# Kernel tuning notes

Hardware: AMD Instinct MI355X
Metric: run time of the kernel (lower is better)

Reference implementation:

```python
import jax, jax.numpy as jnp
import numpy as np

PARENTS = (-1, 0, 0, 0, 1, 2, 3, 4, 5, 6, 7, 8, 9, 9, 9, 12, 13, 14, 16, 17, 18, 19, 20, 21)
NUM_JOINTS = 24
ROT_RANGE = 0.2
SCALE_RANGE = 0.1
CAM_JIT = 0.1
IMG_SIZE = 512.0
EPS = 1e-8


def _rodrigues(axis, angle):
    # axis: [B,3] (will be re-normalized as in the torch code), angle: [B]
    axis = axis / (jnp.linalg.norm(axis, axis=1, keepdims=True) + EPS)
    c = jnp.cos(angle)[:, None, None]
    s = jnp.sin(angle)[:, None, None]
    x, y, z = axis[:, 0], axis[:, 1], axis[:, 2]
    zeros = jnp.zeros_like(x)
    K = jnp.stack([
        jnp.stack([zeros, -z, y], axis=1),
        jnp.stack([z, zeros, -x], axis=1),
        jnp.stack([-y, x, zeros], axis=1),
    ], axis=1)  # [B,3,3]
    I = jnp.eye(3, dtype=axis.dtype)[None]
    outer = axis[:, :, None] * axis[:, None, :]
    return I + s * K + (1.0 - c) * (outer - I)


def setup_inputs() -> dict:
    key = jax.random.key(0)
    ks = jax.random.split(key, 12)
    B, J = 131072, NUM_JOINTS
    return {
        'poses_3d': jax.random.normal(ks[0], (B, J, 3), jnp.float32),
        'rot_mats': jax.random.normal(ks[1], (B, J, 3, 3), jnp.float32),
        'axis': jax.random.normal(ks[2], (B, J, 3), jnp.float32),
        'angle_u': jax.random.uniform(ks[3], (B, J), jnp.float32),
        'scale_u': jax.random.uniform(ks[4], (B, J), jnp.float32),
        'K': jax.random.normal(ks[5], (B, 3, 3), jnp.float32),
        'R': jax.random.normal(ks[6], (B, 3, 3), jnp.float32),
        't': jax.random.normal(ks[7], (B, 3), jnp.float32),
        'focal_u': jax.random.uniform(ks[8], (B, 2), jnp.float32),
        'yaw_u': jax.random.uniform(ks[9], (B,), jnp.float32),
        'pitch_u': jax.random.uniform(ks[10], (B,), jnp.float32),
        't_jit': jax.random.normal(ks[11], (B, 3), jnp.float32),
    }


def reference(poses_3d, rot_mats, axis, angle_u, scale_u, K, R, t, focal_u, yaw_u, pitch_u, t_jit):
    poses = poses_3d
    rots = rot_mats
    # sequential kinematic-tree walk (parents[i] < i, so already-updated parents feed children)
    for i in range(1, NUM_JOINTS):
        p = PARENTS[i]
        bone = poses[:, i] - poses[:, p]                                   # [B,3]
        blen = jnp.linalg.norm(bone, axis=1, keepdims=True)
        ax = axis[:, i]
        ax = ax / (jnp.linalg.norm(ax, axis=1, keepdims=True) + EPS)       # first normalization (forward)
        ang = (angle_u[:, i] * 2.0 - 1.0) * ROT_RANGE
        Ra = _rodrigues(ax, ang)                                           # [B,3,3]
        rb = jnp.einsum('bij,bj->bi', Ra, bone)
        scale = 1.0 + (scale_u[:, i:i + 1] * 2.0 - 1.0) * SCALE_RANGE
        nb = rb * scale * blen / (jnp.linalg.norm(rb, axis=1, keepdims=True) + EPS)
        poses = poses.at[:, i].set(poses[:, p] + nb)
        rots = rots.at[:, i].set(jnp.einsum('bij,bjk->bik', rots[:, i], Ra))

    # camera jitter
    fs = 1.0 + (focal_u * 2.0 - 1.0) * CAM_JIT * 0.1                       # [B,2]
    K_aug = K.at[:, 0, 0].set(K[:, 0, 0] * fs[:, 0]).at[:, 1, 1].set(K[:, 1, 1] * fs[:, 1])
    yaw = (yaw_u * 2.0 - 1.0) * CAM_JIT * 0.1
    pitch = (pitch_u * 2.0 - 1.0) * CAM_JIT * 0.05
    cy, sy = jnp.cos(yaw), jnp.sin(yaw)
    cp, sp = jnp.cos(pitch), jnp.sin(pitch)
    z = jnp.zeros_like(cy)
    o = jnp.ones_like(cy)
    R_yaw = jnp.stack([jnp.stack([cy, z, sy], 1), jnp.stack([z, o, z], 1), jnp.stack([-sy, z, cy], 1)], 1)
    R_pitch = jnp.stack([jnp.stack([o, z, z], 1), jnp.stack([z, cp, -sp], 1), jnp.stack([z, sp, cp], 1)], 1)
    R_aug = jnp.einsum('bij,bjk->bik', R, jnp.einsum('bij,bjk->bik', R_yaw, R_pitch))
    t_aug = t + t_jit * CAM_JIT * 0.05

    # project and normalize
    cam = jnp.einsum('bij,bnj->bni', R_aug, poses) + t_aug[:, None, :]     # [B,J,3]
    zc = jnp.maximum(cam[:, :, 2], 1e-5)
    u = K_aug[:, 0, 0][:, None] * (cam[:, :, 0] / zc) + K_aug[:, 0, 2][:, None]
    v = K_aug[:, 1, 1][:, None] * (cam[:, :, 1] / zc) + K_aug[:, 1, 2][:, None]
    poses_2d = jnp.stack([u, v], axis=2) / IMG_SIZE * 2.0 - 1.0

    return poses, poses_2d, rots, K_aug, R_aug, t_aug
```

## Files before the change

### kernel.cpp

```cpp
#include <hip/hip_runtime.h>

#define NJ 24
#define EPSF 1e-8f

static __device__ __forceinline__ int parent_of(int i) {
    constexpr int P[NJ] = {-1, 0, 0, 0, 1, 2, 3, 4, 5, 6, 7, 8, 9, 9, 9, 12, 13, 14, 16, 17, 18, 19, 20, 21};
    return P[i];
}

static __device__ __forceinline__ void make_Ra(float ax, float ay, float az, float au, float R[9]) {
    float n1 = sqrtf(ax*ax + ay*ay + az*az) + EPSF;
    ax /= n1; ay /= n1; az /= n1;
    float n2 = sqrtf(ax*ax + ay*ay + az*az) + EPSF;
    ax /= n2; ay /= n2; az /= n2;
    float ang = (au * 2.0f - 1.0f) * 0.2f;
    float c = cosf(ang), s = sinf(ang), oc = 1.0f - c;
    R[0] = 1.0f + oc*(ax*ax - 1.0f); R[1] = -s*az + oc*ax*ay;        R[2] =  s*ay + oc*ax*az;
    R[3] =  s*az + oc*ax*ay;         R[4] = 1.0f + oc*(ay*ay - 1.0f); R[5] = -s*ax + oc*ay*az;
    R[6] = -s*ay + oc*ax*az;         R[7] =  s*ax + oc*ay*az;         R[8] = 1.0f + oc*(az*az - 1.0f);
}

__global__ __launch_bounds__(64)
void poseaug_fused_kernel(const float* __restrict__ poses_3d,
                          const float* __restrict__ rot_mats,
                          const float* __restrict__ axis,
                          const float* __restrict__ angle_u,
                          const float* __restrict__ scale_u,
                          const float* __restrict__ Kin,
                          const float* __restrict__ Rin,
                          const float* __restrict__ tin,
                          const float* __restrict__ focal_u,
                          const float* __restrict__ yaw_u,
                          const float* __restrict__ pitch_u,
                          const float* __restrict__ t_jit,
                          float* __restrict__ out, int B)
{
    __shared__ __align__(16) float stg[64 * 73];
    __shared__ __align__(16) float rbuf[64 * 73];
    const int l  = threadIdx.x;
    const int e0 = blockIdx.x * 64;
    const int n  = min(64, B - e0);
    const int b  = e0 + l;
    const bool act = (b < B);

    float* out_poses = out;
    float* out_2d    = out + (size_t)B * 72;
    float* out_rots  = out + (size_t)B * 120;
    float* out_K     = out + (size_t)B * 336;
    float* out_R     = out + (size_t)B * 345;
    float* out_t     = out + (size_t)B * 354;

    {
        const float* gp = poses_3d + (size_t)e0 * 72;
        const float* ga = axis     + (size_t)e0 * 72;
        if (n == 64) {
            const float4* gp4 = (const float4*)gp;
            const float4* ga4 = (const float4*)ga;
            #pragma unroll
            for (int it = 0; it < 18; ++it) {
                int i4 = l + it * 64;
                float4 vp = gp4[i4];
                float4 va = ga4[i4];
                int o = i4 * 4;
                int base = (o / 72) * 73 + (o % 72);
                rbuf[base] = vp.x; rbuf[base+1] = vp.y; rbuf[base+2] = vp.z; rbuf[base+3] = vp.w;
                stg[base]  = va.x; stg[base+1]  = va.y; stg[base+2]  = va.z; stg[base+3]  = va.w;
            }
        } else {
            for (int o = l; o < n * 72; o += 64) {
                int base = (o / 72) * 73 + (o % 72);
                rbuf[base] = gp[o];
                stg[base]  = ga[o];
            }
        }
    }
    __syncthreads();
    float pf[72];
    #pragma unroll
    for (int k = 0; k < 72; ++k) pf[k] = rbuf[l * 73 + k];

    float au[24], su[24];
    if (act) {
        const float4* ga = (const float4*)(angle_u + (size_t)b * 24);
        const float4* gs = (const float4*)(scale_u + (size_t)b * 24);
        #pragma unroll
        for (int q = 0; q < 6; ++q) {
            float4 va = ga[q]; au[4*q+0]=va.x; au[4*q+1]=va.y; au[4*q+2]=va.z; au[4*q+3]=va.w;
            float4 vs = gs[q]; su[4*q+0]=vs.x; su[4*q+1]=vs.y; su[4*q+2]=vs.z; su[4*q+3]=vs.w;
        }
    }

    #pragma unroll
    for (int i = 1; i < NJ; ++i) {
        const int par = parent_of(i);
        float bx = pf[3*i+0] - pf[3*par+0];
        float by = pf[3*i+1] - pf[3*par+1];
        float bz = pf[3*i+2] - pf[3*par+2];
        float blen = sqrtf(bx*bx + by*by + bz*bz);

        float Ra[9];
        make_Ra(stg[l*73 + 3*i + 0], stg[l*73 + 3*i + 1], stg[l*73 + 3*i + 2], au[i], Ra);

        float rbx = Ra[0]*bx + Ra[1]*by + Ra[2]*bz;
        float rby = Ra[3]*bx + Ra[4]*by + Ra[5]*bz;
        float rbz = Ra[6]*bx + Ra[7]*by + Ra[8]*bz;

        float scale = 1.0f + (su[i] * 2.0f - 1.0f) * 0.1f;
        float rn = sqrtf(rbx*rbx + rby*rby + rbz*rbz) + EPSF;
        float f = scale * blen / rn;

        pf[3*i+0] = pf[3*par+0] + rbx * f;
        pf[3*i+1] = pf[3*par+1] + rby * f;
        pf[3*i+2] = pf[3*par+2] + rbz * f;
    }

    float K00, K02, K11, K12;
    float A[9], tx = 0.f, ty = 0.f, tz = 0.f;
    if (act) {
        float Kf[9];
        const float* kb = Kin + (size_t)b * 9;
        const float* rb = Rin + (size_t)b * 9;
        #pragma unroll
        for (int k = 0; k < 9; ++k) Kf[k] = kb[k];
        float f0 = focal_u[(size_t)b*2+0], f1 = focal_u[(size_t)b*2+1];
        Kf[0] *= 1.0f + (f0*2.0f - 1.0f) * 0.01f;
        Kf[4] *= 1.0f + (f1*2.0f - 1.0f) * 0.01f;
        K00 = Kf[0]; K02 = Kf[2]; K11 = Kf[4]; K12 = Kf[5];

        float yaw   = (yaw_u[b]   * 2.0f - 1.0f) * 0.01f;
        float pitch = (pitch_u[b] * 2.0f - 1.0f) * 0.005f;
        float cy = cosf(yaw),  sy = sinf(yaw);
        float cp = cosf(pitch), sp = sinf(pitch);
        float M00 = cy,   M01 = sy*sp, M02 = sy*cp;
        float M11 = cp,   M12 = -sp;
        float M20 = -sy,  M21 = cy*sp, M22 = cy*cp;

        float R00=rb[0],R01=rb[1],R02=rb[2],R10=rb[3],R11=rb[4],R12=rb[5],R20=rb[6],R21=rb[7],R22=rb[8];
        A[0] = R00*M00 + R02*M20; A[1] = R00*M01 + R01*M11 + R02*M21; A[2] = R00*M02 + R01*M12 + R02*M22;
        A[3] = R10*M00 + R12*M20; A[4] = R10*M01 + R11*M11 + R12*M21; A[5] = R10*M02 + R11*M12 + R12*M22;
        A[6] = R20*M00 + R22*M20; A[7] = R20*M01 + R21*M11 + R22*M21; A[8] = R20*M02 + R21*M12 + R22*M22;

        tx = tin[(size_t)b*3+0] + t_jit[(size_t)b*3+0] * 0.005f;
        ty = tin[(size_t)b*3+1] + t_jit[(size_t)b*3+1] * 0.005f;
        tz = tin[(size_t)b*3+2] + t_jit[(size_t)b*3+2] * 0.005f;

        float* ok = out_K + (size_t)b * 9;
        #pragma unroll
        for (int k = 0; k < 9; ++k) ok[k] = Kf[k];
        float* orr = out_R + (size_t)b * 9;
        #pragma unroll
        for (int k = 0; k < 9; ++k) orr[k] = A[k];
        float* ot = out_t + (size_t)b * 3;
        ot[0] = tx; ot[1] = ty; ot[2] = tz;
    }

    #pragma unroll
    for (int c = 0; c < 3; ++c) {
        __syncthreads();
        const float* gld = rot_mats + (size_t)e0 * 216 + 72 * c;
        if (n == 64) {
            #pragma unroll
            for (int it = 0; it < 18; ++it) {
                int f = it * 64 + l;
                int r = f / 18;
                int k = (f % 18) * 4;
                const float4 v = *(const float4*)(gld + (size_t)r * 216 + k);
                int base = r * 73 + k;
                rbuf[base] = v.x; rbuf[base+1] = v.y; rbuf[base+2] = v.z; rbuf[base+3] = v.w;
            }
        } else {
            for (int o = l; o < n * 72; o += 64)
                rbuf[(o/72)*73 + (o%72)] = gld[(size_t)(o/72)*216 + (o%72)];
        }
        __syncthreads();
        if (act) {
            #pragma unroll
            for (int jj = 0; jj < 8; ++jj) {
                const int j = c * 8 + jj;
                float m[9];
                #pragma unroll
                for (int q = 0; q < 9; ++q) m[q] = rbuf[l*73 + 9*jj + q];
                float r9[9];
                if (j == 0) {
                    #pragma unroll
                    for (int q = 0; q < 9; ++q) r9[q] = m[q];
                } else {
                    float Ra[9];
                    make_Ra(stg[l*73 + 3*j + 0], stg[l*73 + 3*j + 1], stg[l*73 + 3*j + 2], au[j], Ra);
                    r9[0] = m[0]*Ra[0] + m[1]*Ra[3] + m[2]*Ra[6];
                    r9[1] = m[0]*Ra[1] + m[1]*Ra[4] + m[2]*Ra[7];
                    r9[2] = m[0]*Ra[2] + m[1]*Ra[5] + m[2]*Ra[8];
                    r9[3] = m[3]*Ra[0] + m[4]*Ra[3] + m[5]*Ra[6];
                    r9[4] = m[3]*Ra[1] + m[4]*Ra[4] + m[5]*Ra[7];
                    r9[5] = m[3]*Ra[2] + m[4]*Ra[5] + m[5]*Ra[8];
                    r9[6] = m[6]*Ra[0] + m[7]*Ra[3] + m[8]*Ra[6];
                    r9[7] = m[6]*Ra[1] + m[7]*Ra[4] + m[8]*Ra[7];
                    r9[8] = m[6]*Ra[2] + m[7]*Ra[5] + m[8]*Ra[8];
                }
                #pragma unroll
                for (int q = 0; q < 9; ++q) rbuf[l*73 + 9*jj + q] = r9[q];
            }
        }
        __syncthreads();
        float* gst = out_rots + (size_t)e0 * 216 + 72 * c;
        if (n == 64) {
            #pragma unroll
            for (int it = 0; it < 18; ++it) {
                int f = it * 64 + l;
                int r = f / 18;
                int k = (f % 18) * 4;
                int base = r * 73 + k;
                *(float4*)(gst + (size_t)r * 216 + k) =
                    make_float4(rbuf[base], rbuf[base+1], rbuf[base+2], rbuf[base+3]);
            }
        } else {
            for (int o = l; o < n * 72; o += 64)
                gst[(size_t)(o/72)*216 + (o%72)] = rbuf[(o/72)*73 + (o%72)];
        }
    }

    __syncthreads();
    #pragma unroll
    for (int k = 0; k < 72; ++k) stg[l * 73 + k] = pf[k];
    __syncthreads();
    {
        float* g = out_poses + (size_t)e0 * 72;
        if (n == 64) {
            float4* g4 = (float4*)g;
            #pragma unroll
            for (int it = 0; it < 18; ++it) {
                int i4 = l + it * 64;
                int o = i4 * 4;
                int base = (o / 72) * 73 + (o % 72);
                g4[i4] = make_float4(stg[base], stg[base+1], stg[base+2], stg[base+3]);
            }
        } else {
            for (int o = l; o < n * 72; o += 64) g[o] = stg[(o / 72) * 73 + (o % 72)];
        }
    }

    __syncthreads();
    if (act) {
        #pragma unroll
        for (int j = 0; j < NJ; ++j) {
            float px = pf[3*j+0], py = pf[3*j+1], pz = pf[3*j+2];
            float cx = A[0]*px + A[1]*py + A[2]*pz + tx;
            float cv = A[3]*px + A[4]*py + A[5]*pz + ty;
            float cz = A[6]*px + A[7]*py + A[8]*pz + tz;
            float zc = fmaxf(cz, 1e-5f);
            stg[l*73 + 2*j + 0] = (K00 * (cx / zc) + K02) * (2.0f / 512.0f) - 1.0f;
            stg[l*73 + 2*j + 1] = (K11 * (cv / zc) + K12) * (2.0f / 512.0f) - 1.0f;
        }
    }
    __syncthreads();
    {
        float* g = out_2d + (size_t)e0 * 48;
        if (n == 64) {
            float4* g4 = (float4*)g;
            #pragma unroll
            for (int it = 0; it < 12; ++it) {
                int i4 = l + it * 64;
                int o = i4 * 4;
                int base = (o / 48) * 73 + (o % 48);
                g4[i4] = make_float4(stg[base], stg[base+1], stg[base+2], stg[base+3]);
            }
        } else {
            for (int o = l; o < n * 48; o += 64) g[o] = stg[(o / 48) * 73 + (o % 48)];
        }
    }
}

extern "C" void kernel_launch(void* const* d_in, const int* in_sizes, int n_in,
                              void* d_out, int out_size, void* d_ws, size_t ws_size,
                              hipStream_t stream) {
    const float* poses_3d = (const float*)d_in[0];
    const float* rot_mats = (const float*)d_in[1];
    const float* axis     = (const float*)d_in[2];
    const float* angle_u  = (const float*)d_in[3];
    const float* scale_u  = (const float*)d_in[4];
    const float* Kin      = (const float*)d_in[5];
    const float* Rin      = (const float*)d_in[6];
    const float* tin      = (const float*)d_in[7];
    const float* focal_u  = (const float*)d_in[8];
    const float* yaw_u    = (const float*)d_in[9];
    const float* pitch_u  = (const float*)d_in[10];
    const float* t_jit    = (const float*)d_in[11];
    float* out = (float*)d_out;

    const int B = in_sizes[9];

    dim3 blk(64), grd((B + 63) / 64);
    hipLaunchKernelGGL(poseaug_fused_kernel, grd, blk, 0, stream,
                       poses_3d, rot_mats, axis, angle_u, scale_u, Kin, Rin, tin,
                       focal_u, yaw_u, pitch_u, t_jit, out, B);
}
```

Before: 484.8 us.

## Fuse kinematic walk into rot-mat chunks and drop second shared buffer

```diff
diff --git a/kernel.cpp b/kernel.cpp
--- a/kernel.cpp
+++ b/kernel.cpp
@@ -20,22 +20,21 @@
     R[6] = -s*ay + oc*ax*az;         R[7] =  s*ax + oc*ay*az;         R[8] = 1.0f + oc*(az*az - 1.0f);
 }
 
-__global__ __launch_bounds__(64)
-void poseaug_fused_kernel(const float* __restrict__ poses_3d,
-                          const float* __restrict__ rot_mats,
-                          const float* __restrict__ axis,
-                          const float* __restrict__ angle_u,
-                          const float* __restrict__ scale_u,
-                          const float* __restrict__ Kin,
-                          const float* __restrict__ Rin,
-                          const float* __restrict__ tin,
-                          const float* __restrict__ focal_u,
-                          const float* __restrict__ yaw_u,
-                          const float* __restrict__ pitch_u,
-                          const float* __restrict__ t_jit,
-                          float* __restrict__ out, int B)
+__global__ __launch_bounds__(64, 2)
+void poseaug_fused2_kernel(const float* __restrict__ poses_3d,
+                           const float* __restrict__ rot_mats,
+                           const float* __restrict__ axis,
+                           const float* __restrict__ angle_u,
+                           const float* __restrict__ scale_u,
+                           const float* __restrict__ Kin,
+                           const float* __restrict__ Rin,
+                           const float* __restrict__ tin,
+                           const float* __restrict__ focal_u,
+                           const float* __restrict__ yaw_u,
+                           const float* __restrict__ pitch_u,
+                           const float* __restrict__ t_jit,
+                           float* __restrict__ out, int B)
 {
-    __shared__ __align__(16) float stg[64 * 73];
     __shared__ __align__(16) float rbuf[64 * 73];
     const int l  = threadIdx.x;
     const int e0 = blockIdx.x * 64;
@@ -50,112 +49,32 @@
     float* out_R     = out + (size_t)B * 345;
     float* out_t     = out + (size_t)B * 354;
 
-    {
-        const float* gp = poses_3d + (size_t)e0 * 72;
-        const float* ga = axis     + (size_t)e0 * 72;
-        if (n == 64) {
-            const float4* gp4 = (const float4*)gp;
-            const float4* ga4 = (const float4*)ga;
-            #pragma unroll
-            for (int it = 0; it < 18; ++it) {
-                int i4 = l + it * 64;
-                float4 vp = gp4[i4];
-                float4 va = ga4[i4];
-                int o = i4 * 4;
-                int base = (o / 72) * 73 + (o % 72);
-                rbuf[base] = vp.x; rbuf[base+1] = vp.y; rbuf[base+2] = vp.z; rbuf[base+3] = vp.w;
-                stg[base]  = va.x; stg[base+1]  = va.y; stg[base+2]  = va.z; stg[base+3]  = va.w;
-            }
-        } else {
-            for (int o = l; o < n * 72; o += 64) {
-                int base = (o / 72) * 73 + (o % 72);
-                rbuf[base] = gp[o];
-                stg[base]  = ga[o];
-            }
-        }
-    }
-    __syncthreads();
     float pf[72];
-    #pragma unroll
-    for (int k = 0; k < 72; ++k) pf[k] = rbuf[l * 73 + k];
-
-    float au[24], su[24];
-    if (act) {
-        const float4* ga = (const float4*)(angle_u + (size_t)b * 24);
-        const float4* gs = (const float4*)(scale_u + (size_t)b * 24);
-        #pragma unroll
-        for (int q = 0; q < 6; ++q) {
-            float4 va = ga[q]; au[4*q+0]=va.x; au[4*q+1]=va.y; au[4*q+2]=va.z; au[4*q+3]=va.w;
-            float4 vs = gs[q]; su[4*q+0]=vs.x; su[4*q+1]=vs.y; su[4*q+2]=vs.z; su[4*q+3]=vs.w;
-        }
-    }
-
-    #pragma unroll
-    for (int i = 1; i < NJ; ++i) {
-        const int par = parent_of(i);
-        float bx = pf[3*i+0] - pf[3*par+0];
-        float by = pf[3*i+1] - pf[3*par+1];
-        float bz = pf[3*i+2] - pf[3*par+2];
-        float blen = sqrtf(bx*bx + by*by + bz*bz);
-
-        float Ra[9];
-        make_Ra(stg[l*73 + 3*i + 0], stg[l*73 + 3*i + 1], stg[l*73 + 3*i + 2], au[i], Ra);
-
-        float rbx = Ra[0]*bx + Ra[1]*by + Ra[2]*bz;
-        float rby = Ra[3]*bx + Ra[4]*by + Ra[5]*bz;
-        float rbz = Ra[6]*bx + Ra[7]*by + Ra[8]*bz;
-
-        float scale = 1.0f + (su[i] * 2.0f - 1.0f) * 0.1f;
-        float rn = sqrtf(rbx*rbx + rby*rby + rbz*rbz) + EPSF;
-        float f = scale * blen / rn;
-
-        pf[3*i+0] = pf[3*par+0] + rbx * f;
-        pf[3*i+1] = pf[3*par+1] + rby * f;
-        pf[3*i+2] = pf[3*par+2] + rbz * f;
-    }
-
-    float K00, K02, K11, K12;
-    float A[9], tx = 0.f, ty = 0.f, tz = 0.f;
-    if (act) {
-        float Kf[9];
-        const float* kb = Kin + (size_t)b * 9;
-        const float* rb = Rin + (size_t)b * 9;
-        #pragma unroll
-        for (int k = 0; k < 9; ++k) Kf[k] = kb[k];
-        float f0 = focal_u[(size_t)b*2+0], f1 = focal_u[(size_t)b*2+1];
-        Kf[0] *= 1.0f + (f0*2.0f - 1.0f) * 0.01f;
-        Kf[4] *= 1.0f + (f1*2.0f - 1.0f) * 0.01f;
-        K00 = Kf[0]; K02 = Kf[2]; K11 = Kf[4]; K12 = Kf[5];
-
-        float yaw   = (yaw_u[b]   * 2.0f - 1.0f) * 0.01f;
-        float pitch = (pitch_u[b] * 2.0f - 1.0f) * 0.005f;
-        float cy = cosf(yaw),  sy = sinf(yaw);
-        float cp = cosf(pitch), sp = sinf(pitch);
-        float M00 = cy,   M01 = sy*sp, M02 = sy*cp;
-        float M11 = cp,   M12 = -sp;
-        float M20 = -sy,  M21 = cy*sp, M22 = cy*cp;
-
-        float R00=rb[0],R01=rb[1],R02=rb[2],R10=rb[3],R11=rb[4],R12=rb[5],R20=rb[6],R21=rb[7],R22=rb[8];
-        A[0] = R00*M00 + R02*M20; A[1] = R00*M01 + R01*M11 + R02*M21; A[2] = R00*M02 + R01*M12 + R02*M22;
-        A[3] = R10*M00 + R12*M20; A[4] = R10*M01 + R11*M11 + R12*M21; A[5] = R10*M02 + R11*M12 + R12*M22;
-        A[6] = R20*M00 + R22*M20; A[7] = R20*M01 + R21*M11 + R22*M21; A[8] = R20*M02 + R21*M12 + R22*M22;
-
-        tx = tin[(size_t)b*3+0] + t_jit[(size_t)b*3+0] * 0.005f;
-        ty = tin[(size_t)b*3+1] + t_jit[(size_t)b*3+1] * 0.005f;
-        tz = tin[(size_t)b*3+2] + t_jit[(size_t)b*3+2] * 0.005f;
-
-        float* ok = out_K + (size_t)b * 9;
-        #pragma unroll
-        for (int k = 0; k < 9; ++k) ok[k] = Kf[k];
-        float* orr = out_R + (size_t)b * 9;
-        #pragma unroll
-        for (int k = 0; k < 9; ++k) orr[k] = A[k];
-        float* ot = out_t + (size_t)b * 3;
-        ot[0] = tx; ot[1] = ty; ot[2] = tz;
-    }
 
     #pragma unroll
     for (int c = 0; c < 3; ++c) {
+        float axl[24], au8[8], su8[8];
+        if (act) {
+            const float4* gp = (const float4*)(poses_3d + (size_t)b * 72 + 24 * c);
+            const float4* ga = (const float4*)(axis     + (size_t)b * 72 + 24 * c);
+            #pragma unroll
+            for (int q = 0; q < 6; ++q) {
+                float4 vp = gp[q];
+                pf[24*c + 4*q + 0] = vp.x; pf[24*c + 4*q + 1] = vp.y;
+                pf[24*c + 4*q + 2] = vp.z; pf[24*c + 4*q + 3] = vp.w;
+                float4 va = ga[q];
+                axl[4*q+0] = va.x; axl[4*q+1] = va.y; axl[4*q+2] = va.z; axl[4*q+3] = va.w;
+            }
+            const float4* gau = (const float4*)(angle_u + (size_t)b * 24 + 8 * c);
+            const float4* gsu = (const float4*)(scale_u + (size_t)b * 24 + 8 * c);
+            float4 a0 = gau[0], a1 = gau[1];
+            au8[0]=a0.x; au8[1]=a0.y; au8[2]=a0.z; au8[3]=a0.w;
+            au8[4]=a1.x; au8[5]=a1.y; au8[6]=a1.z; au8[7]=a1.w;
+            float4 s0 = gsu[0], s1 = gsu[1];
+            su8[0]=s0.x; su8[1]=s0.y; su8[2]=s0.z; su8[3]=s0.w;
+            su8[4]=s1.x; su8[5]=s1.y; su8[6]=s1.z; su8[7]=s1.w;
+        }
+
         __syncthreads();
         const float* gld = rot_mats + (size_t)e0 * 216 + 72 * c;
         if (n == 64) {
@@ -163,20 +82,21 @@
             for (int it = 0; it < 18; ++it) {
                 int f = it * 64 + l;
                 int r = f / 18;
-                int k = (f % 18) * 4;
+                int k = (f - r * 18) * 4;
                 const float4 v = *(const float4*)(gld + (size_t)r * 216 + k);
                 int base = r * 73 + k;
-                rbuf[base] = v.x; rbuf[base+1] = v.y; rbuf[base+2] = v.z; rbuf[base+3] = v.w;
+                rbuf[base+0] = v.x; rbuf[base+1] = v.y; rbuf[base+2] = v.z; rbuf[base+3] = v.w;
             }
         } else {
             for (int o = l; o < n * 72; o += 64)
                 rbuf[(o/72)*73 + (o%72)] = gld[(size_t)(o/72)*216 + (o%72)];
         }
         __syncthreads();
+
         if (act) {
             #pragma unroll
             for (int jj = 0; jj < 8; ++jj) {
-                const int j = c * 8 + jj;
+                const int j = 8 * c + jj;
                 float m[9];
                 #pragma unroll
                 for (int q = 0; q < 9; ++q) m[q] = rbuf[l*73 + 9*jj + q];
@@ -186,7 +106,23 @@
                     for (int q = 0; q < 9; ++q) r9[q] = m[q];
                 } else {
                     float Ra[9];
-                    make_Ra(stg[l*73 + 3*j + 0], stg[l*73 + 3*j + 1], stg[l*73 + 3*j + 2], au[j], Ra);
+                    make_Ra(axl[3*jj+0], axl[3*jj+1], axl[3*jj+2], au8[jj], Ra);
+
+                    const int par = parent_of(j);
+                    float bx = pf[3*j+0] - pf[3*par+0];
+                    float by = pf[3*j+1] - pf[3*par+1];
+                    float bz = pf[3*j+2] - pf[3*par+2];
+                    float blen = sqrtf(bx*bx + by*by + bz*bz);
+                    float rbx = Ra[0]*bx + Ra[1]*by + Ra[2]*bz;
+                    float rby = Ra[3]*bx + Ra[4]*by + Ra[5]*bz;
+                    float rbz = Ra[6]*bx + Ra[7]*by + Ra[8]*bz;
+                    float scale = 1.0f + (su8[jj] * 2.0f - 1.0f) * 0.1f;
+                    float rn = sqrtf(rbx*rbx + rby*rby + rbz*rbz) + EPSF;
+                    float fsc = scale * blen / rn;
+                    pf[3*j+0] = pf[3*par+0] + rbx * fsc;
+                    pf[3*j+1] = pf[3*par+1] + rby * fsc;
+                    pf[3*j+2] = pf[3*par+2] + rbz * fsc;
+
                     r9[0] = m[0]*Ra[0] + m[1]*Ra[3] + m[2]*Ra[6];
                     r9[1] = m[0]*Ra[1] + m[1]*Ra[4] + m[2]*Ra[7];
                     r9[2] = m[0]*Ra[2] + m[1]*Ra[5] + m[2]*Ra[8];
@@ -202,13 +138,14 @@
             }
         }
         __syncthreads();
+
         float* gst = out_rots + (size_t)e0 * 216 + 72 * c;
         if (n == 64) {
             #pragma unroll
             for (int it = 0; it < 18; ++it) {
                 int f = it * 64 + l;
                 int r = f / 18;
-                int k = (f % 18) * 4;
+                int k = (f - r * 18) * 4;
                 int base = r * 73 + k;
                 *(float4*)(gst + (size_t)r * 216 + k) =
                     make_float4(rbuf[base], rbuf[base+1], rbuf[base+2], rbuf[base+3]);
@@ -219,24 +156,44 @@
         }
     }
 
-    __syncthreads();
-    #pragma unroll
-    for (int k = 0; k < 72; ++k) stg[l * 73 + k] = pf[k];
-    __syncthreads();
-    {
-        float* g = out_poses + (size_t)e0 * 72;
-        if (n == 64) {
-            float4* g4 = (float4*)g;
-            #pragma unroll
-            for (int it = 0; it < 18; ++it) {
-                int i4 = l + it * 64;
-                int o = i4 * 4;
-                int base = (o / 72) * 73 + (o % 72);
-                g4[i4] = make_float4(stg[base], stg[base+1], stg[base+2], stg[base+3]);
-            }
-        } else {
-            for (int o = l; o < n * 72; o += 64) g[o] = stg[(o / 72) * 73 + (o % 72)];
-        }
+    float K00, K02, K11, K12;
+    float A[9], tx = 0.f, ty = 0.f, tz = 0.f;
+    if (act) {
+        float Kf[9];
+        const float* kb = Kin + (size_t)b * 9;
+        const float* rb = Rin + (size_t)b * 9;
+        #pragma unroll
+        for (int k = 0; k < 9; ++k) Kf[k] = kb[k];
+        float f0 = focal_u[(size_t)b*2+0], f1 = focal_u[(size_t)b*2+1];
+        Kf[0] *= 1.0f + (f0*2.0f - 1.0f) * 0.01f;
+        Kf[4] *= 1.0f + (f1*2.0f - 1.0f) * 0.01f;
+        K00 = Kf[0]; K02 = Kf[2]; K11 = Kf[4]; K12 = Kf[5];
+
+        float yaw   = (yaw_u[b]   * 2.0f - 1.0f) * 0.01f;
+        float pitch = (pitch_u[b] * 2.0f - 1.0f) * 0.005f;
+        float cy = cosf(yaw),  sy = sinf(yaw);
+        float cp = cosf(pitch), sp = sinf(pitch);
+        float M00 = cy,   M01 = sy*sp, M02 = sy*cp;
+        float M11 = cp,   M12 = -sp;
+        float M20 = -sy,  M21 = cy*sp, M22 = cy*cp;
+
+        float R00=rb[0],R01=rb[1],R02=rb[2],R10=rb[3],R11=rb[4],R12=rb[5],R20=rb[6],R21=rb[7],R22=rb[8];
+        A[0] = R00*M00 + R02*M20; A[1] = R00*M01 + R01*M11 + R02*M21; A[2] = R00*M02 + R01*M12 + R02*M22;
+        A[3] = R10*M00 + R12*M20; A[4] = R10*M01 + R11*M11 + R12*M21; A[5] = R10*M02 + R11*M12 + R12*M22;
+        A[6] = R20*M00 + R22*M20; A[7] = R20*M01 + R21*M11 + R22*M21; A[8] = R20*M02 + R21*M12 + R22*M22;
+
+        tx = tin[(size_t)b*3+0] + t_jit[(size_t)b*3+0] * 0.005f;
+        ty = tin[(size_t)b*3+1] + t_jit[(size_t)b*3+1] * 0.005f;
+        tz = tin[(size_t)b*3+2] + t_jit[(size_t)b*3+2] * 0.005f;
+
+        float* ok = out_K + (size_t)b * 9;
+        #pragma unroll
+        for (int k = 0; k < 9; ++k) ok[k] = Kf[k];
+        float* orr = out_R + (size_t)b * 9;
+        #pragma unroll
+        for (int k = 0; k < 9; ++k) orr[k] = A[k];
+        float* ot = out_t + (size_t)b * 3;
+        ot[0] = tx; ot[1] = ty; ot[2] = tz;
     }
 
     __syncthreads();
@@ -248,8 +205,8 @@
             float cv = A[3]*px + A[4]*py + A[5]*pz + ty;
             float cz = A[6]*px + A[7]*py + A[8]*pz + tz;
             float zc = fmaxf(cz, 1e-5f);
-            stg[l*73 + 2*j + 0] = (K00 * (cx / zc) + K02) * (2.0f / 512.0f) - 1.0f;
-            stg[l*73 + 2*j + 1] = (K11 * (cv / zc) + K12) * (2.0f / 512.0f) - 1.0f;
+            rbuf[l*73 + 2*j + 0] = (K00 * (cx / zc) + K02) * (2.0f / 512.0f) - 1.0f;
+            rbuf[l*73 + 2*j + 1] = (K11 * (cv / zc) + K12) * (2.0f / 512.0f) - 1.0f;
         }
     }
     __syncthreads();
@@ -262,10 +219,32 @@
                 int i4 = l + it * 64;
                 int o = i4 * 4;
                 int base = (o / 48) * 73 + (o % 48);
-                g4[i4] = make_float4(stg[base], stg[base+1], stg[base+2], stg[base+3]);
-            }
-        } else {
-            for (int o = l; o < n * 48; o += 64) g[o] = stg[(o / 48) * 73 + (o % 48)];
+                g4[i4] = make_float4(rbuf[base], rbuf[base+1], rbuf[base+2], rbuf[base+3]);
+            }
+        } else {
+            for (int o = l; o < n * 48; o += 64) g[o] = rbuf[(o / 48) * 73 + (o % 48)];
+        }
+    }
+
+    __syncthreads();
+    if (act) {
+        #pragma unroll
+        for (int k = 0; k < 72; ++k) rbuf[l * 73 + k] = pf[k];
+    }
+    __syncthreads();
+    {
+        float* g = out_poses + (size_t)e0 * 72;
+        if (n == 64) {
+            float4* g4 = (float4*)g;
+            #pragma unroll
+            for (int it = 0; it < 18; ++it) {
+                int i4 = l + it * 64;
+                int o = i4 * 4;
+                int base = (o / 72) * 73 + (o % 72);
+                g4[i4] = make_float4(rbuf[base], rbuf[base+1], rbuf[base+2], rbuf[base+3]);
+            }
+        } else {
+            for (int o = l; o < n * 72; o += 64) g[o] = rbuf[(o / 72) * 73 + (o % 72)];
         }
     }
 }
@@ -290,7 +269,7 @@
     const int B = in_sizes[9];
 
     dim3 blk(64), grd((B + 63) / 64);
-    hipLaunchKernelGGL(poseaug_fused_kernel, grd, blk, 0, stream,
+    hipLaunchKernelGGL(poseaug_fused2_kernel, grd, blk, 0, stream,
                        poses_3d, rot_mats, axis, angle_u, scale_u, Kin, Rin, tin,
                        focal_u, yaw_u, pitch_u, t_jit, out, B);
 }
```

After: 424.7 us. 1.14x faster.
